# Kernel tuning notes

Hardware: AMD Instinct MI355X
Metric: run time of the kernel (lower is better)

The kernel has to match this reference:

```python
import jax, jax.numpy as jnp
import numpy as np

S, X, G = 2048, 2048, 2
INPUT_SIZE = (3, 32, 32)
F = int(np.prod(INPUT_SIZE))


def setup_inputs() -> dict:
    key = jax.random.key(0)
    k1, k2, k3 = jax.random.split(key, 3)
    samples = jax.random.normal(k1, (S,) + INPUT_SIZE, dtype=jnp.float32)
    x = jax.random.normal(k2, (X,) + INPUT_SIZE, dtype=jnp.float32)
    # per-feature std per gradation, kept in [0.1, 1.0) like ranges_std scaling
    std = jax.random.uniform(k3, (G, F), dtype=jnp.float32, minval=0.1, maxval=1.0)
    return {"samples": samples, "x": x, "std": std}


def reference(samples, x, std):
    # samples: [S, C, H, W], x: [X, C, H, W], std: [G, F]
    G_, F_ = std.shape
    s = samples.reshape(samples.shape[0], F_)  # [S, F]
    xf = x.reshape(x.shape[0], F_)             # [X, F]
    w = 1.0 / (std * std)                       # [G, F] precision
    # per-gradation normalizer: -0.5*F*log(2pi) - sum_f log(std)
    const = -0.5 * F_ * jnp.log(2.0 * jnp.pi) - jnp.sum(jnp.log(std), axis=1)  # [G]
    # sum_f -0.5*((s-x)/std)^2 expanded: -0.5*(s^2 w - 2 s w x + x^2 w)
    A = jnp.einsum('sf,gf->gs', s * s, w)        # [G, S]
    C = jnp.einsum('xf,gf->gx', xf * xf, w)      # [G, X]
    B = jnp.einsum('sf,gf,xf->gsx', s, w, xf)    # [G, S, X] cross term
    logits = -0.5 * (A[:, :, None] - 2.0 * B + C[:, None, :]) + const[:, None, None]
    lp = jax.nn.logsumexp(logits, axis=2)        # over x (mixture components)
    lp = jax.nn.logsumexp(lp, axis=0)            # over gradations
    return lp - jnp.log(jnp.float32(x.shape[0] * G_))
```

## Files before the change

kernel.cpp:

```cpp
#include <hip/hip_runtime.h>
#include <math.h>

#define S_N 2048
#define X_N 2048
#define G_N 2
#define F_N 3072

#define TM 128
#define TN 128
#define BK 32

typedef __bf16 bf16;
typedef __bf16 bf16x4 __attribute__((ext_vector_type(4)));
typedef __bf16 bf16x8 __attribute__((ext_vector_type(8)));
typedef float f32x4 __attribute__((ext_vector_type(4)));

__global__ void k_const(const float* __restrict__ stdv, float* __restrict__ constg) {
  int g = blockIdx.x;
  int t = threadIdx.x;
  float s = 0.f;
  for (int f = t; f < F_N; f += 256) s += logf(stdv[g * F_N + f]);
  for (int o = 32; o; o >>= 1) s += __shfl_xor(s, o);
  __shared__ float red[4];
  int w = t >> 6, l = t & 63;
  if (l == 0) red[w] = s;
  __syncthreads();
  if (t == 0) {
    float tot = red[0] + red[1] + red[2] + red[3];
    constg[g] = -0.5f * (float)F_N * 1.8378770664093453f - tot;
  }
}

__global__ void k_prep(const float* __restrict__ samples, const float* __restrict__ xin,
                       const float* __restrict__ stdv,
                       bf16* __restrict__ U, bf16* __restrict__ V,
                       float* __restrict__ A, float* __restrict__ C) {
  int r = blockIdx.x;
  int t = threadIdx.x;
  bool isS = (r < S_N);
  const float* src = isS ? (samples + (size_t)r * F_N) : (xin + (size_t)(r - S_N) * F_N);
  float4 row[3];
#pragma unroll
  for (int j = 0; j < 3; ++j) row[j] = ((const float4*)src)[t + j * 256];

  __shared__ float red[4];
  int w = t >> 6, l = t & 63;

  for (int g = 0; g < G_N; ++g) {
    const float4* sd = (const float4*)(stdv + (size_t)g * F_N);
    bf16* dst = isS ? (U + ((size_t)g * S_N + r) * F_N)
                    : (V + ((size_t)g * X_N + (r - S_N)) * F_N);
    float acc = 0.f;
#pragma unroll
    for (int j = 0; j < 3; ++j) {
      float4 d = sd[t + j * 256];
      float u0 = row[j].x / d.x;
      float u1 = row[j].y / d.y;
      float u2 = row[j].z / d.z;
      float u3 = row[j].w / d.w;
      bf16x4 b;
      b[0] = (bf16)u0; b[1] = (bf16)u1; b[2] = (bf16)u2; b[3] = (bf16)u3;
      float f0 = (float)b[0], f1 = (float)b[1], f2 = (float)b[2], f3 = (float)b[3];
      acc += f0 * f0 + f1 * f1 + f2 * f2 + f3 * f3;
      ((bf16x4*)dst)[t + j * 256] = b;
    }
    for (int o = 32; o; o >>= 1) acc += __shfl_xor(acc, o);
    __syncthreads();
    if (l == 0) red[w] = acc;
    __syncthreads();
    if (t == 0) {
      float tot = red[0] + red[1] + red[2] + red[3];
      if (isS) A[(size_t)g * S_N + r] = tot;
      else     C[(size_t)g * X_N + (r - S_N)] = tot;
    }
  }
}

__global__ __launch_bounds__(256) void k_gemm(const bf16* __restrict__ U, const bf16* __restrict__ V,
                                              const float* __restrict__ A, const float* __restrict__ C,
                                              float* __restrict__ logits) {
  __shared__ bf16 ldsA[TM * BK];
  __shared__ bf16 ldsB[TN * BK];

  int t = threadIdx.x;
  int g = blockIdx.z;
  int bm = blockIdx.y * TM;
  int bn = blockIdx.x * TN;

  const bf16* Ub = U + ((size_t)g * S_N + bm) * F_N;
  const bf16* Vb = V + ((size_t)g * X_N + bn) * F_N;

  int wave = t >> 6, lane = t & 63;
  int wm = wave & 1, wn = wave >> 1;
  int r = lane & 15, q = lane >> 4;
  int sq = q ^ (r & 3);

  int c0 = t, c1 = t + 256;
  int row0 = c0 >> 2, gc0 = (c0 & 3) ^ (row0 & 3);
  int row1 = c1 >> 2, gc1 = (c1 & 3) ^ (row1 & 3);
  const bf16* gA0 = Ub + (size_t)row0 * F_N + gc0 * 8;
  const bf16* gA1 = Ub + (size_t)row1 * F_N + gc1 * 8;
  const bf16* gB0 = Vb + (size_t)row0 * F_N + gc0 * 8;
  const bf16* gB1 = Vb + (size_t)row1 * F_N + gc1 * 8;
  bf16* lA0 = ldsA + c0 * 8;
  bf16* lA1 = ldsA + c1 * 8;
  bf16* lB0 = ldsB + c0 * 8;
  bf16* lB1 = ldsB + c1 * 8;

  f32x4 acc[4][4] = {};

  int abase = (wm * 64 + r) * BK + sq * 8;
  int bbase = (wn * 64 + r) * BK + sq * 8;

  for (int k0 = 0; k0 < F_N; k0 += BK) {
    __syncthreads();
    __builtin_amdgcn_global_load_lds((const __attribute__((address_space(1))) void*)(gA0 + k0),
                                     (__attribute__((address_space(3))) void*)lA0, 16, 0, 0);
    __builtin_amdgcn_global_load_lds((const __attribute__((address_space(1))) void*)(gA1 + k0),
                                     (__attribute__((address_space(3))) void*)lA1, 16, 0, 0);
    __builtin_amdgcn_global_load_lds((const __attribute__((address_space(1))) void*)(gB0 + k0),
                                     (__attribute__((address_space(3))) void*)lB0, 16, 0, 0);
    __builtin_amdgcn_global_load_lds((const __attribute__((address_space(1))) void*)(gB1 + k0),
                                     (__attribute__((address_space(3))) void*)lB1, 16, 0, 0);
    __syncthreads();

    bf16x8 af[4], bfr[4];
#pragma unroll
    for (int mi = 0; mi < 4; ++mi) af[mi] = *(const bf16x8*)(ldsA + abase + mi * 16 * BK);
#pragma unroll
    for (int ni = 0; ni < 4; ++ni) bfr[ni] = *(const bf16x8*)(ldsB + bbase + ni * 16 * BK);

#pragma unroll
    for (int mi = 0; mi < 4; ++mi)
#pragma unroll
      for (int ni = 0; ni < 4; ++ni)
        acc[mi][ni] = __builtin_amdgcn_mfma_f32_16x16x32_bf16(af[mi], bfr[ni], acc[mi][ni], 0, 0, 0);
  }

  const float* Ap = A + (size_t)g * S_N + bm + wm * 64;
  const float* Cp = C + (size_t)g * X_N + bn + wn * 64;
  float cv[4];
#pragma unroll
  for (int ni = 0; ni < 4; ++ni) cv[ni] = Cp[ni * 16 + r];
#pragma unroll
  for (int mi = 0; mi < 4; ++mi) {
#pragma unroll
    for (int i = 0; i < 4; ++i) {
      int rowl = wm * 64 + mi * 16 + q * 4 + i;
      float av = Ap[mi * 16 + q * 4 + i];
      float* orow = logits + ((size_t)g * S_N + bm + rowl) * X_N + bn + wn * 64;
#pragma unroll
      for (int ni = 0; ni < 4; ++ni)
        orow[ni * 16 + r] = acc[mi][ni][i] - 0.5f * (av + cv[ni]);
    }
  }
}

__global__ void k_lse(const float* __restrict__ logits, const float* __restrict__ constg,
                      float* __restrict__ out) {
  int s = blockIdx.x, t = threadIdx.x;
  float c0 = constg[0], c1 = constg[1];
  const float4* p0 = (const float4*)(logits + (size_t)s * X_N);
  const float4* p1 = (const float4*)(logits + ((size_t)S_N + s) * X_N);
  float4 v[4];
  v[0] = p0[t]; v[1] = p0[t + 256];
  v[2] = p1[t]; v[3] = p1[t + 256];
  v[0].x += c0; v[0].y += c0; v[0].z += c0; v[0].w += c0;
  v[1].x += c0; v[1].y += c0; v[1].z += c0; v[1].w += c0;
  v[2].x += c1; v[2].y += c1; v[2].z += c1; v[2].w += c1;
  v[3].x += c1; v[3].y += c1; v[3].z += c1; v[3].w += c1;

  float m = v[0].x;
#pragma unroll
  for (int j = 0; j < 4; ++j) {
    m = fmaxf(m, v[j].x); m = fmaxf(m, v[j].y);
    m = fmaxf(m, v[j].z); m = fmaxf(m, v[j].w);
  }
  for (int o = 32; o; o >>= 1) m = fmaxf(m, __shfl_xor(m, o));
  __shared__ float redm[4];
  __shared__ float reds[4];
  int w = t >> 6, l = t & 63;
  if (l == 0) redm[w] = m;
  __syncthreads();
  m = fmaxf(fmaxf(redm[0], redm[1]), fmaxf(redm[2], redm[3]));

  float sum = 0.f;
#pragma unroll
  for (int j = 0; j < 4; ++j) {
    sum += expf(v[j].x - m) + expf(v[j].y - m) + expf(v[j].z - m) + expf(v[j].w - m);
  }
  for (int o = 32; o; o >>= 1) sum += __shfl_xor(sum, o);
  if (l == 0) reds[w] = sum;
  __syncthreads();
  if (t == 0) {
    float tot = reds[0] + reds[1] + reds[2] + reds[3];
    out[s] = m + logf(tot) - 8.317766166719343f;
  }
}

extern "C" void kernel_launch(void* const* d_in, const int* in_sizes, int n_in,
                              void* d_out, int out_size, void* d_ws, size_t ws_size,
                              hipStream_t stream) {
  const float* samples = (const float*)d_in[0];
  const float* xin     = (const float*)d_in[1];
  const float* stdv    = (const float*)d_in[2];
  float* out = (float*)d_out;

  char* ws = (char*)d_ws;
  size_t off = 0;
  bf16* U = (bf16*)(ws + off);       off += (size_t)G_N * S_N * F_N * 2;
  bf16* V = (bf16*)(ws + off);       off += (size_t)G_N * X_N * F_N * 2;
  float* logits = (float*)(ws + off); off += (size_t)G_N * S_N * X_N * 4;
  float* A = (float*)(ws + off);     off += (size_t)G_N * S_N * 4;
  float* C = (float*)(ws + off);     off += (size_t)G_N * X_N * 4;
  float* constg = (float*)(ws + off); off += 256;

  k_const<<<dim3(G_N), dim3(256), 0, stream>>>(stdv, constg);
  k_prep<<<dim3(S_N + X_N), dim3(256), 0, stream>>>(samples, xin, stdv, U, V, A, C);
  k_gemm<<<dim3(X_N / TN, S_N / TM, G_N), dim3(256), 0, stream>>>(U, V, A, C, logits);
  k_lse<<<dim3(S_N), dim3(256), 0, stream>>>(logits, constg, out);
}
```

Measured before the change: 175.9 us.

## Double-buffer GEMM LDS tiles with register-staged prefetch two steps ahead

```diff
diff --git a/kernel.cpp b/kernel.cpp
--- a/kernel.cpp
+++ b/kernel.cpp
@@ -9,11 +9,14 @@
 #define TM 128
 #define TN 128
 #define BK 32
+#define ITERS (F_N / BK)
 
 typedef __bf16 bf16;
 typedef __bf16 bf16x4 __attribute__((ext_vector_type(4)));
 typedef __bf16 bf16x8 __attribute__((ext_vector_type(8)));
 typedef float f32x4 __attribute__((ext_vector_type(4)));
+
+#define WAIT_LGKM0() __builtin_amdgcn_s_waitcnt(0xc07f)
 
 __global__ void k_const(const float* __restrict__ stdv, float* __restrict__ constg) {
   int g = blockIdx.x;
@@ -79,8 +82,8 @@
 __global__ __launch_bounds__(256) void k_gemm(const bf16* __restrict__ U, const bf16* __restrict__ V,
                                               const float* __restrict__ A, const float* __restrict__ C,
                                               float* __restrict__ logits) {
-  __shared__ bf16 ldsA[TM * BK];
-  __shared__ bf16 ldsB[TN * BK];
+  __shared__ bf16 ldsA[2][TM * BK];
+  __shared__ bf16 ldsB[2][TN * BK];
 
   int t = threadIdx.x;
   int g = blockIdx.z;
@@ -93,48 +96,60 @@
   int wave = t >> 6, lane = t & 63;
   int wm = wave & 1, wn = wave >> 1;
   int r = lane & 15, q = lane >> 4;
-  int sq = q ^ (r & 3);
+  int sq = q ^ ((r >> 1) & 3);
 
   int c0 = t, c1 = t + 256;
-  int row0 = c0 >> 2, gc0 = (c0 & 3) ^ (row0 & 3);
-  int row1 = c1 >> 2, gc1 = (c1 & 3) ^ (row1 & 3);
+  int row0 = c0 >> 2, gc0 = (c0 & 3) ^ ((row0 >> 1) & 3);
+  int row1 = c1 >> 2, gc1 = (c1 & 3) ^ ((row1 >> 1) & 3);
   const bf16* gA0 = Ub + (size_t)row0 * F_N + gc0 * 8;
   const bf16* gA1 = Ub + (size_t)row1 * F_N + gc1 * 8;
   const bf16* gB0 = Vb + (size_t)row0 * F_N + gc0 * 8;
   const bf16* gB1 = Vb + (size_t)row1 * F_N + gc1 * 8;
-  bf16* lA0 = ldsA + c0 * 8;
-  bf16* lA1 = ldsA + c1 * 8;
-  bf16* lB0 = ldsB + c0 * 8;
-  bf16* lB1 = ldsB + c1 * 8;
 
   f32x4 acc[4][4] = {};
-
   int abase = (wm * 64 + r) * BK + sq * 8;
   int bbase = (wn * 64 + r) * BK + sq * 8;
 
-  for (int k0 = 0; k0 < F_N; k0 += BK) {
-    __syncthreads();
-    __builtin_amdgcn_global_load_lds((const __attribute__((address_space(1))) void*)(gA0 + k0),
-                                     (__attribute__((address_space(3))) void*)lA0, 16, 0, 0);
-    __builtin_amdgcn_global_load_lds((const __attribute__((address_space(1))) void*)(gA1 + k0),
-                                     (__attribute__((address_space(3))) void*)lA1, 16, 0, 0);
-    __builtin_amdgcn_global_load_lds((const __attribute__((address_space(1))) void*)(gB0 + k0),
-                                     (__attribute__((address_space(3))) void*)lB0, 16, 0, 0);
-    __builtin_amdgcn_global_load_lds((const __attribute__((address_space(1))) void*)(gB1 + k0),
-                                     (__attribute__((address_space(3))) void*)lB1, 16, 0, 0);
-    __syncthreads();
+  bf16x8 sA0[2], sA1[2], sB0[2], sB1[2];
+
+  sA0[0] = *(const bf16x8*)(gA0);      sA1[0] = *(const bf16x8*)(gA1);
+  sB0[0] = *(const bf16x8*)(gB0);      sB1[0] = *(const bf16x8*)(gB1);
+  sA0[1] = *(const bf16x8*)(gA0 + BK); sA1[1] = *(const bf16x8*)(gA1 + BK);
+  sB0[1] = *(const bf16x8*)(gB0 + BK); sB1[1] = *(const bf16x8*)(gB1 + BK);
+  *(bf16x8*)(&ldsA[0][c0 * 8]) = sA0[0];
+  *(bf16x8*)(&ldsA[0][c1 * 8]) = sA1[0];
+  *(bf16x8*)(&ldsB[0][c0 * 8]) = sB0[0];
+  *(bf16x8*)(&ldsB[0][c1 * 8]) = sB1[0];
+  WAIT_LGKM0();
+  __builtin_amdgcn_s_barrier();
+
+  for (int it = 0; it < ITERS; ++it) {
+    int b = it & 1, nb = b ^ 1;
+    int pk = (it + 2) * BK;
+    sA0[b] = *(const bf16x8*)(gA0 + pk);
+    sA1[b] = *(const bf16x8*)(gA1 + pk);
+    sB0[b] = *(const bf16x8*)(gB0 + pk);
+    sB1[b] = *(const bf16x8*)(gB1 + pk);
 
     bf16x8 af[4], bfr[4];
 #pragma unroll
-    for (int mi = 0; mi < 4; ++mi) af[mi] = *(const bf16x8*)(ldsA + abase + mi * 16 * BK);
-#pragma unroll
-    for (int ni = 0; ni < 4; ++ni) bfr[ni] = *(const bf16x8*)(ldsB + bbase + ni * 16 * BK);
+    for (int mi = 0; mi < 4; ++mi) af[mi] = *(const bf16x8*)(&ldsA[b][abase + mi * 16 * BK]);
+#pragma unroll
+    for (int ni = 0; ni < 4; ++ni) bfr[ni] = *(const bf16x8*)(&ldsB[b][bbase + ni * 16 * BK]);
 
 #pragma unroll
     for (int mi = 0; mi < 4; ++mi)
 #pragma unroll
       for (int ni = 0; ni < 4; ++ni)
         acc[mi][ni] = __builtin_amdgcn_mfma_f32_16x16x32_bf16(af[mi], bfr[ni], acc[mi][ni], 0, 0, 0);
+
+    *(bf16x8*)(&ldsA[nb][c0 * 8]) = sA0[nb];
+    *(bf16x8*)(&ldsA[nb][c1 * 8]) = sA1[nb];
+    *(bf16x8*)(&ldsB[nb][c0 * 8]) = sB0[nb];
+    *(bf16x8*)(&ldsB[nb][c1 * 8]) = sB1[nb];
+
+    WAIT_LGKM0();
+    __builtin_amdgcn_s_barrier();
   }
 
   const float* Ap = A + (size_t)g * S_N + bm + wm * 64;
@@ -208,11 +223,11 @@
 
   char* ws = (char*)d_ws;
   size_t off = 0;
-  bf16* U = (bf16*)(ws + off);       off += (size_t)G_N * S_N * F_N * 2;
-  bf16* V = (bf16*)(ws + off);       off += (size_t)G_N * X_N * F_N * 2;
+  bf16* U = (bf16*)(ws + off);        off += (size_t)G_N * S_N * F_N * 2;
+  bf16* V = (bf16*)(ws + off);        off += (size_t)G_N * X_N * F_N * 2;
   float* logits = (float*)(ws + off); off += (size_t)G_N * S_N * X_N * 4;
-  float* A = (float*)(ws + off);     off += (size_t)G_N * S_N * 4;
-  float* C = (float*)(ws + off);     off += (size_t)G_N * X_N * 4;
+  float* A = (float*)(ws + off);      off += (size_t)G_N * S_N * 4;
+  float* C = (float*)(ws + off);      off += (size_t)G_N * X_N * 4;
   float* constg = (float*)(ws + off); off += 256;
 
   k_const<<<dim3(G_N), dim3(256), 0, stream>>>(stdv, constg);
```

After: 652.4 us. 3.71x slower.
